# Kernel tuning notes

Measured on AMD Instinct MI355X. Metric: run time of the kernel, lower is better.

## Reference

```python
import jax, jax.numpy as jnp
import numpy as np

E, D, H = 16, 768, 768  # experts, d_model, d_hidden (FMoETransformerMLP(16, 768, 768))
B, N = 32, 197


def setup_inputs() -> dict:
    key = jax.random.key(0)
    ks = jax.random.split(key, 7)
    s = 0.02
    return {
        "x": jax.random.normal(ks[0], (B, N, D), dtype=jnp.float32),
        "W1": jax.random.normal(ks[1], (E, H, D), dtype=jnp.float32) * s,
        "b1": jax.random.normal(ks[2], (E, H), dtype=jnp.float32) * s,
        "W2": jax.random.normal(ks[3], (E, D, H), dtype=jnp.float32) * s,
        "b2": jax.random.normal(ks[4], (E, D), dtype=jnp.float32) * s,
        "Wg": jax.random.normal(ks[5], (E, D), dtype=jnp.float32) * s,
        "bg": jnp.zeros((E,), dtype=jnp.float32),
    }


def reference(x, W1, b1, W2, b2, Wg, bg):
    # FMoETransformerMLP forward: flatten tokens, gate, dispatch, expert MLP, combine.
    Bx, Nx, Dx = x.shape
    t = x.reshape(-1, Dx)                     # [T, D] tokens
    logits = t @ Wg.T + bg                    # [T, E] gate logits
    idx = jnp.argmax(logits, axis=-1)
    out = jnp.zeros_like(t)
    for e in range(W1.shape[0]):              # small fixed expert loop
        mask = (idx == e).astype(t.dtype)[:, None]
        h = jax.nn.gelu(t @ W1[e].T + b1[e], approximate=False)  # htoh4 + GELU
        y = h @ W2[e].T + b2[e]                                   # h4toh
        out = out + mask * y
    return out.reshape(Bx, Nx, Dx)
```

## Files before the change

### kernel.cpp

```cpp
#include <hip/hip_runtime.h>
#include <hip/hip_bf16.h>
#include <math.h>
#include <type_traits>

#define T_TOK 6304
#define DMODEL 768
#define NEXP 16
#define NGATE 394

typedef __bf16 bf16x8 __attribute__((ext_vector_type(8)));
typedef float f32x4 __attribute__((ext_vector_type(4)));

__device__ __forceinline__ unsigned short f2bf(float f) {
    __hip_bfloat16 b = __float2bfloat16(f);
    return __builtin_bit_cast(unsigned short, b);
}
__device__ __forceinline__ unsigned int pack2(float lo, float hi) {
    return (unsigned int)f2bf(lo) | ((unsigned int)f2bf(hi) << 16);
}

__global__ __launch_bounds__(256) void gate_kernel(
    const float* __restrict__ x, const float* __restrict__ Wg,
    const float* __restrict__ bg, int* __restrict__ cnt, int* __restrict__ list,
    unsigned short* __restrict__ xb)
{
    __shared__ double lg[16][17];
    const int tt = threadIdx.x >> 4;
    const int e  = threadIdx.x & 15;
    const int t  = blockIdx.x * 16 + tt;
    const float4* xr = (const float4*)(x + (size_t)t * DMODEL);
    const float4* wr = (const float4*)(Wg + (size_t)e * DMODEL);
    double s0 = 0, s1 = 0, s2 = 0, s3 = 0;
#pragma unroll 4
    for (int i = 0; i < DMODEL / 4; ++i) {
        float4 a = xr[i], w = wr[i];
        s0 += (double)a.x * (double)w.x;
        s1 += (double)a.y * (double)w.y;
        s2 += (double)a.z * (double)w.z;
        s3 += (double)a.w * (double)w.w;
    }
    lg[tt][e] = (s0 + s1) + (s2 + s3);
    if (xb) {
        uint4* dst = (uint4*)(xb + (size_t)t * DMODEL + e * 48);
#pragma unroll
        for (int u = 0; u < 6; ++u) {
            float4 a = xr[e * 12 + 2 * u], b = xr[e * 12 + 2 * u + 1];
            dst[u] = make_uint4(pack2(a.x, a.y), pack2(a.z, a.w),
                                pack2(b.x, b.y), pack2(b.z, b.w));
        }
    }
    __syncthreads();
    if (e == 0) {
        double best = -1e300; int bi = 0;
#pragma unroll
        for (int k = 0; k < NEXP; ++k) {
            double v = lg[tt][k] + (double)bg[k];
            if (v > best) { best = v; bi = k; }
        }
        int pos = atomicAdd(&cnt[bi], 1);
        list[bi * T_TOK + pos] = t;
    }
}

template<int GELU, int PACKED_IN, int PACKED_OUT, typename TW, typename TOUT>
__global__ __launch_bounds__(256, 4) void expert_gemm(
    const unsigned short* __restrict__ in, const TW* __restrict__ Wb,
    const float* __restrict__ bias, const int* __restrict__ cnt,
    const int* __restrict__ list, TOUT* __restrict__ outp)
{
    constexpr int BK = 64, LDK = 72;
    constexpr bool W_F32 = std::is_same<TW, float>::value;
    __shared__ __align__(16) unsigned short At[2][64][LDK];
    __shared__ __align__(16) unsigned short Bt[2][64][LDK];
    __shared__ int toks[64];

    const int bx = blockIdx.x;
    const int e = bx / 12, nb = bx % 12;
    const int c = cnt[e];
    int off = 0;
    if (PACKED_IN || PACKED_OUT)
        for (int k = 0; k < e; ++k) off += cnt[k];
    const int n0 = nb * 64;
    const int tid = threadIdx.x, lane = tid & 63, w = tid >> 6;
    const int rg = w & 1, cgp = w >> 1;
    const int l15 = lane & 15, q8 = (lane >> 4) * 8, q = lane >> 4;
    const int sr = tid >> 2, sk = (tid & 3) * 16;

    const TW* bsrc = Wb + (size_t)e * DMODEL * DMODEL + (size_t)(n0 + sr) * DMODEL + sk;
    const int* lst = list + e * T_TOK;

    uint4 pa[2], pb[2];
    float4 fb[4];

    for (int yt = blockIdx.y; yt * 64 < c; yt += 8) {
        const int m0 = yt * 64;
        __syncthreads();
        if (!PACKED_OUT && tid < 64) {
            int mi = m0 + tid;
            toks[tid] = lst[mi < c ? mi : c - 1];
        }
        const int ma0 = m0 + sr;
        const int mac = ma0 < c ? ma0 : c - 1;
        const unsigned short* asrc = PACKED_IN
            ? in + (size_t)(off + mac) * DMODEL + sk
            : in + (size_t)lst[mac] * DMODEL + sk;

        f32x4 acc[2][2];
#pragma unroll
        for (int i = 0; i < 2; ++i)
#pragma unroll
            for (int j = 0; j < 2; ++j) acc[i][j] = (f32x4){0.f, 0.f, 0.f, 0.f};

        auto load_regs = [&](int k0) {
            const uint4* s = (const uint4*)(asrc + k0);
            pa[0] = s[0]; pa[1] = s[1];
            if constexpr (W_F32) {
                const float4* t2 = (const float4*)(bsrc + k0);
                fb[0] = t2[0]; fb[1] = t2[1]; fb[2] = t2[2]; fb[3] = t2[3];
            } else {
                const uint4* t2 = (const uint4*)(bsrc + k0);
                pb[0] = t2[0]; pb[1] = t2[1];
            }
        };
        auto store_tiles = [&](int buf) {
            *(uint4*)&At[buf][sr][sk] = pa[0]; *(uint4*)&At[buf][sr][sk + 8] = pa[1];
            if constexpr (W_F32) {
                uint4 w0, w1;
                w0.x = pack2(fb[0].x, fb[0].y); w0.y = pack2(fb[0].z, fb[0].w);
                w0.z = pack2(fb[1].x, fb[1].y); w0.w = pack2(fb[1].z, fb[1].w);
                w1.x = pack2(fb[2].x, fb[2].y); w1.y = pack2(fb[2].z, fb[2].w);
                w1.z = pack2(fb[3].x, fb[3].y); w1.w = pack2(fb[3].z, fb[3].w);
                *(uint4*)&Bt[buf][sr][sk] = w0; *(uint4*)&Bt[buf][sr][sk + 8] = w1;
            } else {
                *(uint4*)&Bt[buf][sr][sk] = pb[0]; *(uint4*)&Bt[buf][sr][sk + 8] = pb[1];
            }
        };

        load_regs(0);
        store_tiles(0);
#pragma unroll 1
        for (int it = 0; it < DMODEL / BK; ++it) {
            __syncthreads();
            if (it + 1 < DMODEL / BK) load_regs((it + 1) * BK);
            const int buf = it & 1;
#pragma unroll
            for (int kk = 0; kk < BK; kk += 32) {
                bf16x8 a0 = *(const bf16x8*)&At[buf][rg * 32 + l15][kk + q8];
                bf16x8 a1 = *(const bf16x8*)&At[buf][rg * 32 + 16 + l15][kk + q8];
                bf16x8 b0 = *(const bf16x8*)&Bt[buf][cgp * 32 + l15][kk + q8];
                bf16x8 b1 = *(const bf16x8*)&Bt[buf][cgp * 32 + 16 + l15][kk + q8];
                acc[0][0] = __builtin_amdgcn_mfma_f32_16x16x32_bf16(b0, a0, acc[0][0], 0, 0, 0);
                acc[0][1] = __builtin_amdgcn_mfma_f32_16x16x32_bf16(b1, a0, acc[0][1], 0, 0, 0);
                acc[1][0] = __builtin_amdgcn_mfma_f32_16x16x32_bf16(b0, a1, acc[1][0], 0, 0, 0);
                acc[1][1] = __builtin_amdgcn_mfma_f32_16x16x32_bf16(b1, a1, acc[1][1], 0, 0, 0);
            }
            if (it + 1 < DMODEL / BK) store_tiles(buf ^ 1);
        }

#pragma unroll
        for (int i = 0; i < 2; ++i) {
            const int mrow = rg * 32 + i * 16 + l15;
            if (m0 + mrow < c) {
                const size_t rb = PACKED_OUT
                    ? (size_t)(off + m0 + mrow) * DMODEL
                    : (size_t)toks[mrow] * DMODEL;
#pragma unroll
                for (int j = 0; j < 2; ++j) {
                    const int colb = n0 + cgp * 32 + j * 16 + q * 4;
                    const float4 bv = *(const float4*)&bias[e * DMODEL + colb];
                    float v0 = acc[i][j][0] + bv.x;
                    float v1 = acc[i][j][1] + bv.y;
                    float v2 = acc[i][j][2] + bv.z;
                    float v3 = acc[i][j][3] + bv.w;
                    if (GELU) {
                        v0 = 0.5f * v0 * (1.f + erff(v0 * 0.70710678118654752f));
                        v1 = 0.5f * v1 * (1.f + erff(v1 * 0.70710678118654752f));
                        v2 = 0.5f * v2 * (1.f + erff(v2 * 0.70710678118654752f));
                        v3 = 0.5f * v3 * (1.f + erff(v3 * 0.70710678118654752f));
                    }
                    if constexpr (std::is_same<TOUT, float>::value) {
                        *(float4*)&outp[rb + colb] = make_float4(v0, v1, v2, v3);
                    } else {
                        uint2 p; p.x = pack2(v0, v1); p.y = pack2(v2, v3);
                        *(uint2*)&outp[rb + colb] = p;
                    }
                }
            }
        }
    }
}

template<int GELU, typename TA, typename TW, typename TOUT>
__global__ __launch_bounds__(256, 4) void expert_layer(
    const TA* __restrict__ in, const TW* __restrict__ W,
    const float* __restrict__ bias, const int* __restrict__ cnt,
    const int* __restrict__ list, TOUT* __restrict__ outp)
{
    constexpr int BK = 64, LDK = 72;
    constexpr bool A_F32 = std::is_same<TA, float>::value;
    constexpr bool W_F32 = std::is_same<TW, float>::value;
    __shared__ __align__(16) unsigned short At[2][64][LDK];
    __shared__ __align__(16) unsigned short Bt[2][64][LDK];
    __shared__ int toks[64];

    const int bx = blockIdx.x;
    const int e = bx / 12, nb = bx % 12;
    const int c = cnt[e];
    const int n0 = nb * 64;
    const int tid = threadIdx.x, lane = tid & 63, w = tid >> 6;
    const int rg = w & 1, cgp = w >> 1;
    const int l15 = lane & 15, q8 = (lane >> 4) * 8, q = lane >> 4;
    const int sr = tid >> 2, sk = (tid & 3) * 16;

    const TW* bsrc = W + (size_t)e * DMODEL * DMODEL + (size_t)(n0 + sr) * DMODEL + sk;
    const int* lst = list + e * T_TOK;

    uint4 pa[2], pb[2];
    float4 fa[4], fb[4];

    for (int yt = blockIdx.y; yt * 64 < c; yt += 8) {
        const int m0 = yt * 64;
        __syncthreads();
        if (tid < 64) {
            int mi = m0 + tid;
            toks[tid] = lst[mi < c ? mi : c - 1];
        }
        int ma = m0 + sr;
        const TA* asrc = in + (size_t)lst[ma < c ? ma : c - 1] * DMODEL + sk;

        f32x4 acc[2][2];
#pragma unroll
        for (int i = 0; i < 2; ++i)
#pragma unroll
            for (int j = 0; j < 2; ++j) acc[i][j] = (f32x4){0.f, 0.f, 0.f, 0.f};

        auto load_regs = [&](int k0) {
            if constexpr (A_F32) {
                const float4* s = (const float4*)(asrc + k0);
                fa[0] = s[0]; fa[1] = s[1]; fa[2] = s[2]; fa[3] = s[3];
            } else {
                const uint4* s = (const uint4*)(asrc + k0);
                pa[0] = s[0]; pa[1] = s[1];
            }
            if constexpr (W_F32) {
                const float4* s = (const float4*)(bsrc + k0);
                fb[0] = s[0]; fb[1] = s[1]; fb[2] = s[2]; fb[3] = s[3];
            } else {
                const uint4* s = (const uint4*)(bsrc + k0);
                pb[0] = s[0]; pb[1] = s[1];
            }
        };
        auto store_tiles = [&](int buf) {
            if constexpr (A_F32) {
                uint4 w0, w1;
                w0.x = pack2(fa[0].x, fa[0].y); w0.y = pack2(fa[0].z, fa[0].w);
                w0.z = pack2(fa[1].x, fa[1].y); w0.w = pack2(fa[1].z, fa[1].w);
                w1.x = pack2(fa[2].x, fa[2].y); w1.y = pack2(fa[2].z, fa[2].w);
                w1.z = pack2(fa[3].x, fa[3].y); w1.w = pack2(fa[3].z, fa[3].w);
                *(uint4*)&At[buf][sr][sk] = w0; *(uint4*)&At[buf][sr][sk + 8] = w1;
            } else {
                *(uint4*)&At[buf][sr][sk] = pa[0]; *(uint4*)&At[buf][sr][sk + 8] = pa[1];
            }
            if constexpr (W_F32) {
                uint4 w0, w1;
                w0.x = pack2(fb[0].x, fb[0].y); w0.y = pack2(fb[0].z, fb[0].w);
                w0.z = pack2(fb[1].x, fb[1].y); w0.w = pack2(fb[1].z, fb[1].w);
                w1.x = pack2(fb[2].x, fb[2].y); w1.y = pack2(fb[2].z, fb[2].w);
                w1.z = pack2(fb[3].x, fb[3].y); w1.w = pack2(fb[3].z, fb[3].w);
                *(uint4*)&Bt[buf][sr][sk] = w0; *(uint4*)&Bt[buf][sr][sk + 8] = w1;
            } else {
                *(uint4*)&Bt[buf][sr][sk] = pb[0]; *(uint4*)&Bt[buf][sr][sk + 8] = pb[1];
            }
        };

        load_regs(0);
        store_tiles(0);
#pragma unroll 1
        for (int it = 0; it < DMODEL / BK; ++it) {
            __syncthreads();
            if (it + 1 < DMODEL / BK) load_regs((it + 1) * BK);
            const int buf = it & 1;
#pragma unroll
            for (int kk = 0; kk < BK; kk += 32) {
                bf16x8 a0 = *(const bf16x8*)&At[buf][rg * 32 + l15][kk + q8];
                bf16x8 a1 = *(const bf16x8*)&At[buf][rg * 32 + 16 + l15][kk + q8];
                bf16x8 b0 = *(const bf16x8*)&Bt[buf][cgp * 32 + l15][kk + q8];
                bf16x8 b1 = *(const bf16x8*)&Bt[buf][cgp * 32 + 16 + l15][kk + q8];
                acc[0][0] = __builtin_amdgcn_mfma_f32_16x16x32_bf16(a0, b0, acc[0][0], 0, 0, 0);
                acc[0][1] = __builtin_amdgcn_mfma_f32_16x16x32_bf16(a0, b1, acc[0][1], 0, 0, 0);
                acc[1][0] = __builtin_amdgcn_mfma_f32_16x16x32_bf16(a1, b0, acc[1][0], 0, 0, 0);
                acc[1][1] = __builtin_amdgcn_mfma_f32_16x16x32_bf16(a1, b1, acc[1][1], 0, 0, 0);
            }
            if (it + 1 < DMODEL / BK) store_tiles(buf ^ 1);
        }

#pragma unroll
        for (int i = 0; i < 2; ++i) {
#pragma unroll
            for (int j = 0; j < 2; ++j) {
                int col = n0 + cgp * 32 + j * 16 + l15;
                float bv = bias[e * DMODEL + col];
#pragma unroll
                for (int r = 0; r < 4; ++r) {
                    int mrow = rg * 32 + i * 16 + q * 4 + r;
                    if (m0 + mrow < c) {
                        float val = acc[i][j][r] + bv;
                        if (GELU) val = 0.5f * val * (1.f + erff(val * 0.70710678118654752f));
                        size_t idx = (size_t)toks[mrow] * DMODEL + col;
                        if constexpr (std::is_same<TOUT, float>::value) outp[idx] = val;
                        else outp[idx] = f2bf(val);
                    }
                }
            }
        }
    }
}

extern "C" void kernel_launch(void* const* d_in, const int* in_sizes, int n_in,
                              void* d_out, int out_size, void* d_ws, size_t ws_size,
                              hipStream_t stream)
{
    const float* x  = (const float*)d_in[0];
    const float* W1 = (const float*)d_in[1];
    const float* b1 = (const float*)d_in[2];
    const float* W2 = (const float*)d_in[3];
    const float* b2 = (const float*)d_in[4];
    const float* Wg = (const float*)d_in[5];
    const float* bg = (const float*)d_in[6];
    float* out = (float*)d_out;

    char* ws   = (char*)d_ws;
    int*  cnt  = (int*)ws;
    int*  list = (int*)(ws + 256);
    unsigned short* xb  = (unsigned short*)(ws + 403712);
    unsigned short* h   = (unsigned short*)(ws + 10086656);
    const bool big = ws_size >= (size_t)19769600;

    hipMemsetAsync(cnt, 0, 256, stream);
    dim3 grid(12 * NEXP, 8);
    if (big) {
        gate_kernel<<<dim3(NGATE), dim3(256), 0, stream>>>(
            x, Wg, bg, cnt, list, xb);
        expert_gemm<1, 0, 1, float, unsigned short>
            <<<grid, dim3(256), 0, stream>>>(xb, W1, b1, cnt, list, h);
        expert_gemm<0, 1, 0, float, float>
            <<<grid, dim3(256), 0, stream>>>(h, W2, b2, cnt, list, out);
    } else {
        gate_kernel<<<dim3(NGATE), dim3(256), 0, stream>>>(
            x, Wg, bg, cnt, list, nullptr);
        expert_layer<1, float, float, unsigned short>
            <<<grid, dim3(256), 0, stream>>>(x, W1, b1, cnt, list, h);
        expert_layer<0, unsigned short, float, float>
            <<<grid, dim3(256), 0, stream>>>(h, W2, b2, cnt, list, out);
    }
}
```

Baseline: 323.5 us.

## Split gate dot products across threads and stage GEMM epilogue through LDS

The gate kernel now handles 4 tokens per block instead of 16 and splits each token-expert dot product across 4 threads with a shared-memory reduction. This gives about 1576 blocks instead of 394, raising parallelism for the fp64 gate work. The bf16 conversion of x is now done by 48 threads per token with contiguous stores. The expert GEMM epilogue writes bias/GELU results into an LDS tile (reusing the A buffer) and then emits wide row-contiguous stores, trading an extra barrier and LDS pass for better-coalesced global writes of scattered token rows.

```diff
diff --git a/kernel.cpp b/kernel.cpp
--- a/kernel.cpp
+++ b/kernel.cpp
@@ -6,7 +6,7 @@
 #define T_TOK 6304
 #define DMODEL 768
 #define NEXP 16
-#define NGATE 394
+#define GTOK 4
 
 typedef __bf16 bf16x8 __attribute__((ext_vector_type(8)));
 typedef float f32x4 __attribute__((ext_vector_type(4)));
@@ -24,33 +24,44 @@
     const float* __restrict__ bg, int* __restrict__ cnt, int* __restrict__ list,
     unsigned short* __restrict__ xb)
 {
-    __shared__ double lg[16][17];
-    const int tt = threadIdx.x >> 4;
-    const int e  = threadIdx.x & 15;
-    const int t  = blockIdx.x * 16 + tt;
+    __shared__ double part[GTOK][16][5];
+    __shared__ double lg[GTOK][17];
+    const int tid = threadIdx.x;
+    const int tt = tid >> 6;
+    const int e  = (tid >> 2) & 15;
+    const int ks = tid & 3;
+    const int t  = blockIdx.x * GTOK + tt;
     const float4* xr = (const float4*)(x + (size_t)t * DMODEL);
     const float4* wr = (const float4*)(Wg + (size_t)e * DMODEL);
     double s0 = 0, s1 = 0, s2 = 0, s3 = 0;
 #pragma unroll 4
-    for (int i = 0; i < DMODEL / 4; ++i) {
+    for (int ii = 0; ii < 48; ++ii) {
+        const int i = ks * 48 + ii;
         float4 a = xr[i], w = wr[i];
         s0 += (double)a.x * (double)w.x;
         s1 += (double)a.y * (double)w.y;
         s2 += (double)a.z * (double)w.z;
         s3 += (double)a.w * (double)w.w;
     }
-    lg[tt][e] = (s0 + s1) + (s2 + s3);
-    if (xb) {
-        uint4* dst = (uint4*)(xb + (size_t)t * DMODEL + e * 48);
-#pragma unroll
-        for (int u = 0; u < 6; ++u) {
-            float4 a = xr[e * 12 + 2 * u], b = xr[e * 12 + 2 * u + 1];
-            dst[u] = make_uint4(pack2(a.x, a.y), pack2(a.z, a.w),
-                                pack2(b.x, b.y), pack2(b.z, b.w));
-        }
+    part[tt][e][ks] = (s0 + s1) + (s2 + s3);
+    const int u = tid & 63;
+    if (xb && u < 48) {
+        uint4* dst = (uint4*)(xb + (size_t)t * DMODEL);
+        float4 a = xr[4 * u], b = xr[4 * u + 1];
+        float4 c2 = xr[4 * u + 2], d2 = xr[4 * u + 3];
+        dst[2 * u]     = make_uint4(pack2(a.x, a.y), pack2(a.z, a.w),
+                                    pack2(b.x, b.y), pack2(b.z, b.w));
+        dst[2 * u + 1] = make_uint4(pack2(c2.x, c2.y), pack2(c2.z, c2.w),
+                                    pack2(d2.x, d2.y), pack2(d2.z, d2.w));
     }
     __syncthreads();
-    if (e == 0) {
+    if (ks == 0) {
+        double p0 = part[tt][e][0], p1 = part[tt][e][1];
+        double p2 = part[tt][e][2], p3 = part[tt][e][3];
+        lg[tt][e] = (p0 + p1) + (p2 + p3);
+    }
+    __syncthreads();
+    if (u == 0) {
         double best = -1e300; int bi = 0;
 #pragma unroll
         for (int k = 0; k < NEXP; ++k) {
@@ -157,33 +168,49 @@
             if (it + 1 < DMODEL / BK) store_tiles(buf ^ 1);
         }
 
+        __syncthreads();
+        float (*C)[68] = reinterpret_cast<float (*)[68]>(&At[0][0][0]);
 #pragma unroll
         for (int i = 0; i < 2; ++i) {
             const int mrow = rg * 32 + i * 16 + l15;
-            if (m0 + mrow < c) {
+#pragma unroll
+            for (int j = 0; j < 2; ++j) {
+                const int lc = cgp * 32 + j * 16 + q * 4;
+                const float4 bv = *(const float4*)&bias[e * DMODEL + n0 + lc];
+                float v0 = acc[i][j][0] + bv.x;
+                float v1 = acc[i][j][1] + bv.y;
+                float v2 = acc[i][j][2] + bv.z;
+                float v3 = acc[i][j][3] + bv.w;
+                if (GELU) {
+                    v0 = 0.5f * v0 * (1.f + erff(v0 * 0.70710678118654752f));
+                    v1 = 0.5f * v1 * (1.f + erff(v1 * 0.70710678118654752f));
+                    v2 = 0.5f * v2 * (1.f + erff(v2 * 0.70710678118654752f));
+                    v3 = 0.5f * v3 * (1.f + erff(v3 * 0.70710678118654752f));
+                }
+                *(float4*)&C[mrow][lc] = make_float4(v0, v1, v2, v3);
+            }
+        }
+        __syncthreads();
+        {
+            const int row = tid >> 2, q2 = tid & 3;
+            if (m0 + row < c) {
                 const size_t rb = PACKED_OUT
-                    ? (size_t)(off + m0 + mrow) * DMODEL
-                    : (size_t)toks[mrow] * DMODEL;
-#pragma unroll
-                for (int j = 0; j < 2; ++j) {
-                    const int colb = n0 + cgp * 32 + j * 16 + q * 4;
-                    const float4 bv = *(const float4*)&bias[e * DMODEL + colb];
-                    float v0 = acc[i][j][0] + bv.x;
-                    float v1 = acc[i][j][1] + bv.y;
-                    float v2 = acc[i][j][2] + bv.z;
-                    float v3 = acc[i][j][3] + bv.w;
-                    if (GELU) {
-                        v0 = 0.5f * v0 * (1.f + erff(v0 * 0.70710678118654752f));
-                        v1 = 0.5f * v1 * (1.f + erff(v1 * 0.70710678118654752f));
-                        v2 = 0.5f * v2 * (1.f + erff(v2 * 0.70710678118654752f));
-                        v3 = 0.5f * v3 * (1.f + erff(v3 * 0.70710678118654752f));
-                    }
-                    if constexpr (std::is_same<TOUT, float>::value) {
-                        *(float4*)&outp[rb + colb] = make_float4(v0, v1, v2, v3);
-                    } else {
-                        uint2 p; p.x = pack2(v0, v1); p.y = pack2(v2, v3);
-                        *(uint2*)&outp[rb + colb] = p;
-                    }
+                    ? (size_t)(off + m0 + row) * DMODEL
+                    : (size_t)toks[row] * DMODEL;
+                const int cg0 = q2 * 16;
+                const float* cr = &C[row][cg0];
+                if constexpr (std::is_same<TOUT, float>::value) {
+                    float4* dst = (float4*)&outp[rb + n0 + cg0];
+                    dst[0] = *(const float4*)&cr[0];
+                    dst[1] = *(const float4*)&cr[4];
+                    dst[2] = *(const float4*)&cr[8];
+                    dst[3] = *(const float4*)&cr[12];
+                } else {
+                    uint4* dst = (uint4*)&outp[rb + n0 + cg0];
+                    dst[0] = make_uint4(pack2(cr[0], cr[1]),  pack2(cr[2], cr[3]),
+                                        pack2(cr[4], cr[5]),  pack2(cr[6], cr[7]));
+                    dst[1] = make_uint4(pack2(cr[8], cr[9]),  pack2(cr[10], cr[11]),
+                                        pack2(cr[12], cr[13]), pack2(cr[14], cr[15]));
                 }
             }
         }
@@ -339,14 +366,14 @@
     hipMemsetAsync(cnt, 0, 256, stream);
     dim3 grid(12 * NEXP, 8);
     if (big) {
-        gate_kernel<<<dim3(NGATE), dim3(256), 0, stream>>>(
+        gate_kernel<<<dim3(T_TOK / GTOK), dim3(256), 0, stream>>>(
             x, Wg, bg, cnt, list, xb);
         expert_gemm<1, 0, 1, float, unsigned short>
             <<<grid, dim3(256), 0, stream>>>(xb, W1, b1, cnt, list, h);
         expert_gemm<0, 1, 0, float, float>
             <<<grid, dim3(256), 0, stream>>>(h, W2, b2, cnt, list, out);
     } else {
-        gate_kernel<<<dim3(NGATE), dim3(256), 0, stream>>>(
+        gate_kernel<<<dim3(T_TOK / GTOK), dim3(256), 0, stream>>>(
             x, Wg, bg, cnt, list, nullptr);
         expert_layer<1, float, float, unsigned short>
             <<<grid, dim3(256), 0, stream>>>(x, W1, b1, cnt, list, h);
```

After: 377.9 us. 16.8% more time.

## Stage gate weights in LDS and stage expert epilogue through shared memory

Applied to the files above, without the earlier changes.

The gate kernel now copies the full gate weight matrix into LDS once per block and reads it from there instead of from global memory, and the inner loop is unrolled further. The expert GEMM epilogue writes its biased and activated tile into shared memory, which reuses the A tile buffer. It then reads it back so that each thread stores 16 contiguous output elements per row, giving wider and more coalesced global writes. This adds extra barriers and LDS traffic, and the gate kernel uses more LDS per block, which may lower occupancy.

```diff
diff --git a/kernel.cpp b/kernel.cpp
--- a/kernel.cpp
+++ b/kernel.cpp
@@ -24,16 +24,29 @@
     const float* __restrict__ bg, int* __restrict__ cnt, int* __restrict__ list,
     unsigned short* __restrict__ xb)
 {
+    __shared__ __align__(16) float wlds[16][772];
     __shared__ double lg[16][17];
-    const int tt = threadIdx.x >> 4;
-    const int e  = threadIdx.x & 15;
+    const int tid = threadIdx.x;
+    {
+        const float4* src = (const float4*)Wg;
+#pragma unroll
+        for (int v = tid, it = 0; it < 12; ++it, v += 256) {
+            float4 wv = src[v];
+            int row = v / 192, col = (v - row * 192) * 4;
+            *(float4*)&wlds[row][col] = wv;
+        }
+    }
+    __syncthreads();
+
+    const int tt = tid >> 4;
+    const int e  = tid & 15;
     const int t  = blockIdx.x * 16 + tt;
     const float4* xr = (const float4*)(x + (size_t)t * DMODEL);
-    const float4* wr = (const float4*)(Wg + (size_t)e * DMODEL);
     double s0 = 0, s1 = 0, s2 = 0, s3 = 0;
-#pragma unroll 4
+#pragma unroll 8
     for (int i = 0; i < DMODEL / 4; ++i) {
-        float4 a = xr[i], w = wr[i];
+        float4 a = xr[i];
+        float4 w = *(const float4*)&wlds[e][i * 4];
         s0 += (double)a.x * (double)w.x;
         s1 += (double)a.y * (double)w.y;
         s2 += (double)a.z * (double)w.z;
@@ -157,33 +170,49 @@
             if (it + 1 < DMODEL / BK) store_tiles(buf ^ 1);
         }
 
+        __syncthreads();
+        float (*C)[68] = reinterpret_cast<float (*)[68]>(&At[0][0][0]);
 #pragma unroll
         for (int i = 0; i < 2; ++i) {
             const int mrow = rg * 32 + i * 16 + l15;
-            if (m0 + mrow < c) {
+#pragma unroll
+            for (int j = 0; j < 2; ++j) {
+                const int lc = cgp * 32 + j * 16 + q * 4;
+                const float4 bv = *(const float4*)&bias[e * DMODEL + n0 + lc];
+                float v0 = acc[i][j][0] + bv.x;
+                float v1 = acc[i][j][1] + bv.y;
+                float v2 = acc[i][j][2] + bv.z;
+                float v3 = acc[i][j][3] + bv.w;
+                if (GELU) {
+                    v0 = 0.5f * v0 * (1.f + erff(v0 * 0.70710678118654752f));
+                    v1 = 0.5f * v1 * (1.f + erff(v1 * 0.70710678118654752f));
+                    v2 = 0.5f * v2 * (1.f + erff(v2 * 0.70710678118654752f));
+                    v3 = 0.5f * v3 * (1.f + erff(v3 * 0.70710678118654752f));
+                }
+                *(float4*)&C[mrow][lc] = make_float4(v0, v1, v2, v3);
+            }
+        }
+        __syncthreads();
+        {
+            const int row = tid >> 2, q2 = tid & 3;
+            if (m0 + row < c) {
                 const size_t rb = PACKED_OUT
-                    ? (size_t)(off + m0 + mrow) * DMODEL
-                    : (size_t)toks[mrow] * DMODEL;
-#pragma unroll
-                for (int j = 0; j < 2; ++j) {
-                    const int colb = n0 + cgp * 32 + j * 16 + q * 4;
-                    const float4 bv = *(const float4*)&bias[e * DMODEL + colb];
-                    float v0 = acc[i][j][0] + bv.x;
-                    float v1 = acc[i][j][1] + bv.y;
-                    float v2 = acc[i][j][2] + bv.z;
-                    float v3 = acc[i][j][3] + bv.w;
-                    if (GELU) {
-                        v0 = 0.5f * v0 * (1.f + erff(v0 * 0.70710678118654752f));
-                        v1 = 0.5f * v1 * (1.f + erff(v1 * 0.70710678118654752f));
-                        v2 = 0.5f * v2 * (1.f + erff(v2 * 0.70710678118654752f));
-                        v3 = 0.5f * v3 * (1.f + erff(v3 * 0.70710678118654752f));
-                    }
-                    if constexpr (std::is_same<TOUT, float>::value) {
-                        *(float4*)&outp[rb + colb] = make_float4(v0, v1, v2, v3);
-                    } else {
-                        uint2 p; p.x = pack2(v0, v1); p.y = pack2(v2, v3);
-                        *(uint2*)&outp[rb + colb] = p;
-                    }
+                    ? (size_t)(off + m0 + row) * DMODEL
+                    : (size_t)toks[row] * DMODEL;
+                const int cg0 = q2 * 16;
+                const float* cr = &C[row][cg0];
+                if constexpr (std::is_same<TOUT, float>::value) {
+                    float4* dst = (float4*)&outp[rb + n0 + cg0];
+                    dst[0] = *(const float4*)&cr[0];
+                    dst[1] = *(const float4*)&cr[4];
+                    dst[2] = *(const float4*)&cr[8];
+                    dst[3] = *(const float4*)&cr[12];
+                } else {
+                    uint4* dst = (uint4*)&outp[rb + n0 + cg0];
+                    dst[0] = make_uint4(pack2(cr[0], cr[1]),  pack2(cr[2], cr[3]),
+                                        pack2(cr[4], cr[5]),  pack2(cr[6], cr[7]));
+                    dst[1] = make_uint4(pack2(cr[8], cr[9]),  pack2(cr[10], cr[11]),
+                                        pack2(cr[12], cr[13]), pack2(cr[14], cr[15]));
                 }
             }
         }
```

Measured after the change: 292.8 us. -9.5%, faster.
